# Performance work log

Measured on AMD Instinct MI355X. Metric: run time of the kernel, lower is better.

## Reference

```python
import jax, jax.numpy as jnp
import numpy as np
from jax import lax


def setup_inputs() -> dict:
    key = jax.random.key(0)
    k1, k2, k3, k4 = jax.random.split(key, 4)
    N, T = 4096, 64          # num_nodes, tokens per node
    V, H, L = 30000, 256, 2  # vocab, hidden size, LSTM layers
    data = jax.random.randint(k1, (N, T), 0, V, dtype=jnp.int64)
    embed = jax.random.uniform(k2, (V, H), jnp.float32, -0.1, 0.1)
    Wx = jax.random.normal(k3, (L, H, 4 * H), jnp.float32) * 0.05
    Wh = jax.random.normal(k4, (L, H, 4 * H), jnp.float32) * 0.05
    b = jnp.zeros((L, 4 * H), jnp.float32)
    return {"data": data, "embed": embed, "Wx": Wx, "Wh": Wh, "b": b}


def _stacked_lstm_last(tok, Wx, Wh, b):
    # tok: [N, T, H]; Wx/Wh: [L, H, 4H]; b: [L, 4H]
    L, H = Wx.shape[0], Wx.shape[1]
    N = tok.shape[0]
    xs = jnp.swapaxes(tok, 0, 1)  # [T, N, H] -- scan over time, batched over nodes
    c0 = jnp.zeros((L, N, H), tok.dtype)
    h0 = jnp.zeros((L, N, H), tok.dtype)

    def step(carry, x_t):
        c, h = carry
        inp = x_t
        new_c, new_h = [], []
        for l in range(L):  # small fixed layer loop
            z = inp @ Wx[l] + h[l] @ Wh[l] + b[l]  # [N, 4H]
            i, f, g, o = jnp.split(z, 4, axis=-1)   # flax gate order i, f, g, o
            i, f, o = jax.nn.sigmoid(i), jax.nn.sigmoid(f), jax.nn.sigmoid(o)
            g = jnp.tanh(g)
            cl = f * c[l] + i * g
            hl = o * jnp.tanh(cl)
            new_c.append(cl)
            new_h.append(hl)
            inp = hl  # top layer output feeds next layer
        return (jnp.stack(new_c), jnp.stack(new_h)), None

    (_, hF), _ = lax.scan(step, (c0, h0), xs)
    # result[-1] in the original is the top-layer output at the final step,
    # which equals the final top-layer hidden state.
    return hF[-1]  # [N, H]


def reference(data, embed, Wx, Wh, b):
    tok = embed[data]  # [N, T, H] embedding lookup
    return _stacked_lstm_last(tok, Wx, Wh, b)
```

## Files before the change

kernel.cpp:

```cpp
#include <hip/hip_runtime.h>
#include <hip/hip_bf16.h>

#define TT 64
#define HH 256
#define GG 1024

typedef _Float16 f16;
typedef __attribute__((ext_vector_type(8))) _Float16 f16x8;
typedef __attribute__((ext_vector_type(4))) _Float16 f16x4;
typedef __attribute__((ext_vector_type(4))) float f32x4;

__device__ __forceinline__ float exp2_(float x) { return __builtin_amdgcn_exp2f(x); }
__device__ __forceinline__ float sig_(float x) {
    return __builtin_amdgcn_rcpf(1.0f + exp2_(-1.44269504f * x));
}
__device__ __forceinline__ float tanh_(float x) {
    return 1.0f - 2.0f * __builtin_amdgcn_rcpf(1.0f + exp2_(2.88539008f * x));
}
__device__ __forceinline__ float sigp_(float x) { return 1.0f / (1.0f + __expf(-x)); }
__device__ __forceinline__ float tanhp_(float x) {
    x = fminf(fmaxf(x, -15.0f), 15.0f);
    float e = __expf(-2.0f * x);
    return (1.0f - e) / (1.0f + e);
}

__global__ void pack_weights(const float* __restrict__ Wx, const float* __restrict__ Wh,
                             f16* __restrict__ Wp) {
    int t = blockIdx.x * 256 + threadIdx.x;
    int lane = t & 63;
    int nt = (t >> 6) & 63;
    int kk = (t >> 12) & 15;
    int l = t >> 16;
    int n = nt * 16 + (lane & 15);
    int kbase = kk * 32 + 8 * (lane >> 4);
    const float* src = (kbase < 256) ? (Wx + (size_t)l * HH * GG + (size_t)kbase * GG + n)
                                     : (Wh + (size_t)l * HH * GG + (size_t)(kbase - 256) * GG + n);
    f16x8 v;
#pragma unroll
    for (int j = 0; j < 8; ++j) v[j] = (f16)src[(size_t)j * GG];
    *(f16x8*)(Wp + (size_t)t * 8) = v;
}

__global__ __launch_bounds__(512) void embw_gemm(
    const float* __restrict__ embed, const float* __restrict__ bias,
    const f16* __restrict__ Wp, f16* __restrict__ embW, int vocab)
{
    __shared__ f16 a_lds[32 * HH];
    const int tid = threadIdx.x;
    const int lane = tid & 63;
    const int w = tid >> 6;
    const int arow = lane & 15;
    const int g4 = lane >> 4;
    const int r0 = blockIdx.x * 32;

#pragma unroll
    for (int i = 0; i < 4; ++i) {
        int chunk = tid + i * 512;
        int row = chunk >> 6;
        int c4 = chunk & 63;
        int grow = r0 + row; if (grow >= vocab) grow = vocab - 1;
        float4 v = *(const float4*)(embed + (size_t)grow * HH + c4 * 4);
        int idx = row * HH + ((c4 * 4) ^ ((row & 7) << 3));
        *(f16x4*)&a_lds[idx] = (f16x4){(f16)v.x, (f16)v.y, (f16)v.z, (f16)v.w};
    }
    __syncthreads();

    float breg[8];
#pragma unroll
    for (int tt = 0; tt < 8; ++tt) breg[tt] = bias[(w * 8 + tt) * 16 + arow];

    f32x4 acc[2][8];
#pragma unroll
    for (int mt = 0; mt < 2; ++mt)
#pragma unroll
        for (int tt = 0; tt < 8; ++tt)
            acc[mt][tt] = (f32x4){breg[tt], breg[tt], breg[tt], breg[tt]};

    const f16* wl = Wp + (size_t)lane * 8;
#pragma unroll 2
    for (int kk = 0; kk < 8; ++kk) {
        int sw = (kk * 32 + g4 * 8) ^ ((arow & 7) << 3);
        f16x8 a0 = *(const f16x8*)&a_lds[arow * HH + sw];
        f16x8 a1 = *(const f16x8*)&a_lds[(arow + 16) * HH + sw];
        const f16* wkk = wl + (size_t)kk * 64 * 64 * 8;
#pragma unroll
        for (int tt = 0; tt < 8; ++tt) {
            f16x8 b = *(const f16x8*)(wkk + (size_t)(w * 8 + tt) * 64 * 8);
            acc[0][tt] = __builtin_amdgcn_mfma_f32_16x16x32_f16(a0, b, acc[0][tt], 0, 0, 0);
            acc[1][tt] = __builtin_amdgcn_mfma_f32_16x16x32_f16(a1, b, acc[1][tt], 0, 0, 0);
        }
    }

#pragma unroll
    for (int mt = 0; mt < 2; ++mt)
#pragma unroll
        for (int tt = 0; tt < 8; ++tt) {
            int nt = w * 8 + tt;
            int cw = (nt >> 1) & 7;
            int ctt = ((nt >> 4) << 1) | (nt & 1);
#pragma unroll
            for (int r = 0; r < 4; ++r) {
                int row = r0 + mt * 16 + g4 * 4 + r;
                if (row < vocab)
                    embW[(size_t)row * GG + cw * 128 + arow * 8 + ctt] = (f16)acc[mt][tt][r];
            }
        }
}

#define NB2 32
#define LDH 264

__global__ __launch_bounds__(512, 1) void lstm_rec2(
    const int* __restrict__ data, const float* __restrict__ bias,
    const f16* __restrict__ embW, const f16* __restrict__ Wp,
    float* __restrict__ out)
{
    __shared__ f16 h0s[2][NB2 * LDH];
    __shared__ f16 h1s[2][NB2 * LDH];
    __shared__ int toks[NB2 * TT];

    const int tid = threadIdx.x;
    const int lane = tid & 63;
    const int w = tid >> 6;
    const int arow = lane & 15;
    const int g4 = lane >> 4;
    const int n0 = blockIdx.x * NB2;

    for (int i = tid; i < NB2 * LDH; i += 512) {
        h0s[0][i] = (f16)0; h0s[1][i] = (f16)0;
        h1s[0][i] = (f16)0; h1s[1][i] = (f16)0;
    }
    for (int i = tid; i < NB2 * TT; i += 512) toks[i] = data[n0 * TT + i];

    float breg1[8];
#pragma unroll
    for (int tt = 0; tt < 8; ++tt) {
        int col = (tt >> 1) * 256 + w * 32 + (tt & 1) * 16 + arow;
        breg1[tt] = bias[GG + col];
    }

    float c0[16], c1[16];
#pragma unroll
    for (int i = 0; i < 16; ++i) { c0[i] = 0.0f; c1[i] = 0.0f; }

    const f16* wl0 = Wp + (size_t)8 * 64 * 64 * 8 + (size_t)lane * 8;
    const f16* wl1 = Wp + (size_t)16 * 64 * 64 * 8 + (size_t)lane * 8;
    const int zoff = w * 128 + arow * 8;

    int cur0 = 0, cur1 = 0;

    __syncthreads();

#pragma unroll 1
    for (int t = 0; t < TT; ++t) {
        f16x8 zfa0, zfa1, zfa2, zfa3, zfb0, zfb1, zfb2, zfb3;
        {
            int nb = g4 * 4;
            int t0 = toks[(nb + 0) * TT + t];
            int t1 = toks[(nb + 1) * TT + t];
            int t2 = toks[(nb + 2) * TT + t];
            int t3 = toks[(nb + 3) * TT + t];
            zfa0 = *(const f16x8*)(embW + (size_t)t0 * GG + zoff);
            zfa1 = *(const f16x8*)(embW + (size_t)t1 * GG + zoff);
            zfa2 = *(const f16x8*)(embW + (size_t)t2 * GG + zoff);
            zfa3 = *(const f16x8*)(embW + (size_t)t3 * GG + zoff);
        }
        {
            int nb = 16 + g4 * 4;
            int t0 = toks[(nb + 0) * TT + t];
            int t1 = toks[(nb + 1) * TT + t];
            int t2 = toks[(nb + 2) * TT + t];
            int t3 = toks[(nb + 3) * TT + t];
            zfb0 = *(const f16x8*)(embW + (size_t)t0 * GG + zoff);
            zfb1 = *(const f16x8*)(embW + (size_t)t1 * GG + zoff);
            zfb2 = *(const f16x8*)(embW + (size_t)t2 * GG + zoff);
            zfb3 = *(const f16x8*)(embW + (size_t)t3 * GG + zoff);
        }

        f32x4 acc[2][8];
#pragma unroll
        for (int mt = 0; mt < 2; ++mt)
#pragma unroll
            for (int tt = 0; tt < 8; ++tt)
                acc[mt][tt] = (f32x4){0.0f, 0.0f, 0.0f, 0.0f};

        const f16* h0cur = h0s[cur0];
#pragma unroll 2
        for (int kk = 0; kk < 8; ++kk) {
            int k0 = kk * 32 + 8 * g4;
            f16x8 a0 = *(const f16x8*)&h0cur[arow * LDH + k0];
            f16x8 a1 = *(const f16x8*)&h0cur[(arow + 16) * LDH + k0];
            const f16* wkk = wl0 + (size_t)kk * 64 * 64 * 8;
#pragma unroll
            for (int tt = 0; tt < 8; ++tt) {
                int nt = (tt >> 1) * 16 + w * 2 + (tt & 1);
                f16x8 b = *(const f16x8*)(wkk + (size_t)nt * 64 * 8);
                acc[0][tt] = __builtin_amdgcn_mfma_f32_16x16x32_f16(a0, b, acc[0][tt], 0, 0, 0);
                acc[1][tt] = __builtin_amdgcn_mfma_f32_16x16x32_f16(a1, b, acc[1][tt], 0, 0, 0);
            }
        }

#pragma unroll
        for (int tt = 0; tt < 8; ++tt) {
            acc[0][tt][0] += (float)zfa0[tt];
            acc[0][tt][1] += (float)zfa1[tt];
            acc[0][tt][2] += (float)zfa2[tt];
            acc[0][tt][3] += (float)zfa3[tt];
            acc[1][tt][0] += (float)zfb0[tt];
            acc[1][tt][1] += (float)zfb1[tt];
            acc[1][tt][2] += (float)zfb2[tt];
            acc[1][tt][3] += (float)zfb3[tt];
        }

        f16* h0new = h0s[cur0 ^ 1];
#pragma unroll
        for (int mt = 0; mt < 2; ++mt)
#pragma unroll
            for (int sub = 0; sub < 2; ++sub)
#pragma unroll
                for (int r = 0; r < 4; ++r) {
                    int node = mt * 16 + g4 * 4 + r;
                    float i_ = sig_(acc[mt][0 + sub][r]);
                    float f_ = sig_(acc[mt][2 + sub][r]);
                    float g_ = tanh_(acc[mt][4 + sub][r]);
                    float o_ = sig_(acc[mt][6 + sub][r]);
                    int ci = mt * 8 + sub * 4 + r;
                    float c = fmaf(f_, c0[ci], i_ * g_);
                    c0[ci] = c;
                    int u = w * 32 + sub * 16 + arow;
                    h0new[node * LDH + u] = (f16)(o_ * tanh_(c));
                }
        __syncthreads();

        f32x4 acc1[2][8];
#pragma unroll
        for (int mt = 0; mt < 2; ++mt)
#pragma unroll
            for (int tt = 0; tt < 8; ++tt)
                acc1[mt][tt] = (f32x4){breg1[tt], breg1[tt], breg1[tt], breg1[tt]};

        const f16* h1cur = h1s[cur1];
#pragma unroll 4
        for (int kk = 0; kk < 16; ++kk) {
            const f16* asrc = (kk < 8) ? (const f16*)h0new : h1cur;
            int k0 = (kk & 7) * 32 + 8 * g4;
            f16x8 a0 = *(const f16x8*)&asrc[arow * LDH + k0];
            f16x8 a1 = *(const f16x8*)&asrc[(arow + 16) * LDH + k0];
            const f16* wkk = wl1 + (size_t)kk * 64 * 64 * 8;
#pragma unroll
            for (int tt = 0; tt < 8; ++tt) {
                int nt = (tt >> 1) * 16 + w * 2 + (tt & 1);
                f16x8 b = *(const f16x8*)(wkk + (size_t)nt * 64 * 8);
                acc1[0][tt] = __builtin_amdgcn_mfma_f32_16x16x32_f16(a0, b, acc1[0][tt], 0, 0, 0);
                acc1[1][tt] = __builtin_amdgcn_mfma_f32_16x16x32_f16(a1, b, acc1[1][tt], 0, 0, 0);
            }
        }

#pragma unroll
        for (int mt = 0; mt < 2; ++mt)
#pragma unroll
            for (int sub = 0; sub < 2; ++sub)
#pragma unroll
                for (int r = 0; r < 4; ++r) {
                    int node = mt * 16 + g4 * 4 + r;
                    float i_ = sig_(acc1[mt][0 + sub][r]);
                    float f_ = sig_(acc1[mt][2 + sub][r]);
                    float g_ = tanh_(acc1[mt][4 + sub][r]);
                    float o_ = sig_(acc1[mt][6 + sub][r]);
                    int ci = mt * 8 + sub * 4 + r;
                    float c = fmaf(f_, c1[ci], i_ * g_);
                    c1[ci] = c;
                    int u = w * 32 + sub * 16 + arow;
                    h1s[cur1 ^ 1][node * LDH + u] = (f16)(o_ * tanh_(c));
                }
        cur0 ^= 1;
        cur1 ^= 1;
    }
    __syncthreads();

    for (int i = tid; i < NB2 * HH; i += 512) {
        int n = i >> 8, k = i & 255;
        out[(size_t)(n0 + n) * HH + k] = (float)h1s[cur1][n * LDH + k];
    }
}

__global__ void convert_embed(const float* __restrict__ e, f16* __restrict__ o, int n8) {
    int i = blockIdx.x * 256 + threadIdx.x;
    if (i >= n8) return;
    size_t p = (size_t)i * 8;
    float4 a = *(const float4*)(e + p);
    float4 b = *(const float4*)(e + p + 4);
    f16x8 v = { (f16)a.x, (f16)a.y, (f16)a.z, (f16)a.w,
                (f16)b.x, (f16)b.y, (f16)b.z, (f16)b.w };
    *(f16x8*)(o + p) = v;
}

#define FB 32
#define FTH 512
#define FLD 264
__device__ __forceinline__ void fb_layer_step(
    const f16 (*bx)[FLD], f16 (*bh)[FLD], const f16* __restrict__ wlayer,
    const float* breg_l, float* c_l, int lane, int w)
{
    f32x4 acc[2][8];
#pragma unroll
    for (int mt = 0; mt < 2; ++mt)
#pragma unroll
        for (int tt = 0; tt < 8; ++tt) {
            float b = breg_l[tt];
            acc[mt][tt] = (f32x4){b, b, b, b};
        }
    const int arow = lane & 15;
    const int koff = 8 * (lane >> 4);
    const f16* wl = wlayer + (size_t)lane * 8;
#pragma unroll 2
    for (int kk = 0; kk < 16; ++kk) {
        int k0 = (kk & 7) * 32 + koff;
        const f16(*src)[FLD] = (kk < 8) ? bx : (const f16(*)[FLD])bh;
        f16x8 a0 = *(const f16x8*)&src[arow][k0];
        f16x8 a1 = *(const f16x8*)&src[arow + 16][k0];
        const f16* wkk = wl + (size_t)kk * 64 * 64 * 8;
#pragma unroll
        for (int tt = 0; tt < 8; ++tt) {
            int nt = (tt >> 1) * 16 + w * 2 + (tt & 1);
            f16x8 b = *(const f16x8*)(wkk + (size_t)nt * 64 * 8);
            acc[0][tt] = __builtin_amdgcn_mfma_f32_16x16x32_f16(a0, b, acc[0][tt], 0, 0, 0);
            acc[1][tt] = __builtin_amdgcn_mfma_f32_16x16x32_f16(a1, b, acc[1][tt], 0, 0, 0);
        }
    }
    __syncthreads();
#pragma unroll
    for (int mt = 0; mt < 2; ++mt)
#pragma unroll
        for (int sub = 0; sub < 2; ++sub) {
            f32x4 iv = acc[mt][0 + sub], fv = acc[mt][2 + sub];
            f32x4 gv = acc[mt][4 + sub], ov = acc[mt][6 + sub];
#pragma unroll
            for (int r = 0; r < 4; ++r) {
                float i_ = sigp_(iv[r]), f_ = sigp_(fv[r]), g_ = tanhp_(gv[r]), o_ = sigp_(ov[r]);
                int ci = mt * 8 + sub * 4 + r;
                float c = fmaf(f_, c_l[ci], i_ * g_);
                c_l[ci] = c;
                int node = mt * 16 + (lane >> 4) * 4 + r;
                int unit = w * 32 + sub * 16 + (lane & 15);
                bh[node][unit] = (f16)(o_ * tanhp_(c));
            }
        }
    __syncthreads();
}

__global__ __launch_bounds__(FTH, 2) void lstm_mfma_fb(
    const int* __restrict__ data, const float* __restrict__ bias,
    const f16* __restrict__ emb, const f16* __restrict__ Wp,
    float* __restrict__ out, int vocab)
{
    __shared__ f16 x_lds[FB][FLD];
    __shared__ f16 h0_lds[FB][FLD];
    __shared__ f16 h1_lds[FB][FLD];
    const int tid = threadIdx.x;
    const int lane = tid & 63;
    const int w = tid >> 6;
    const int n0 = blockIdx.x * FB;
    for (int i = tid; i < FB * FLD; i += FTH) {
        (&h0_lds[0][0])[i] = (f16)0.0f; (&h1_lds[0][0])[i] = (f16)0.0f;
    }
    float breg[2][8];
#pragma unroll
    for (int l = 0; l < 2; ++l)
#pragma unroll
        for (int tt = 0; tt < 8; ++tt) {
            int col = (tt >> 1) * 256 + w * 32 + (tt & 1) * 16 + (lane & 15);
            breg[l][tt] = bias[l * GG + col];
        }
    float cst[2][16];
#pragma unroll
    for (int i = 0; i < 32; ++i) (&cst[0][0])[i] = 0.0f;
    __syncthreads();
    const f16* Wp0 = Wp;
    const f16* Wp1 = Wp + (size_t)16 * 64 * 64 * 8;
    for (int t = 0; t < TT; ++t) {
        {
            int n = tid >> 4;
            int cg = (tid & 15) * 16;
            int row = data[(n0 + n) * TT + t];
            row = min(max(row, 0), vocab - 1);
            const f16* src = emb + (size_t)row * HH + cg;
            *(f16x8*)&x_lds[n][cg] = *(const f16x8*)src;
            *(f16x8*)&x_lds[n][cg + 8] = *(const f16x8*)(src + 8);
        }
        __syncthreads();
        fb_layer_step(x_lds, h0_lds, Wp0, breg[0], cst[0], lane, w);
        fb_layer_step((const f16(*)[FLD])h0_lds, h1_lds, Wp1, breg[1], cst[1], lane, w);
    }
    for (int i = tid; i < FB * HH; i += FTH) {
        int n = i >> 8, k = i & 255;
        out[(size_t)(n0 + n) * HH + k] = (float)h1_lds[n][k];
    }
}

extern "C" void kernel_launch(void* const* d_in, const int* in_sizes, int n_in,
                              void* d_out, int out_size, void* d_ws, size_t ws_size,
                              hipStream_t stream) {
    const int* data = (const int*)d_in[0];
    const float* embed = (const float*)d_in[1];
    const float* Wx = (const float*)d_in[2];
    const float* Wh = (const float*)d_in[3];
    const float* bias = (const float*)d_in[4];
    float* out = (float*)d_out;
    const int vocab = in_sizes[1] / HH;
    const int nNodes = in_sizes[0] / TT;

    const size_t wp_bytes = (size_t)2 * 16 * 64 * 64 * 8 * 2;
    const size_t embw_bytes = (size_t)vocab * GG * 2;
    const size_t emb16_bytes = (size_t)vocab * HH * 2;

    if (ws_size >= embw_bytes + wp_bytes) {
        f16* embW = (f16*)d_ws;
        f16* Wp = (f16*)((char*)d_ws + embw_bytes);
        pack_weights<<<dim3(512), dim3(256), 0, stream>>>(Wx, Wh, Wp);
        embw_gemm<<<dim3((vocab + 31) / 32), dim3(512), 0, stream>>>(embed, bias, Wp, embW, vocab);
        lstm_rec2<<<dim3(nNodes / NB2), dim3(512), 0, stream>>>(data, bias, embW, Wp, out);
        return;
    }
    f16* emb_h = (f16*)d_ws;
    f16* Wp = (f16*)((char*)d_ws + emb16_bytes);
    int n8 = in_sizes[1] / 8;
    convert_embed<<<dim3((n8 + 255) / 256), dim3(256), 0, stream>>>(embed, emb_h, n8);
    pack_weights<<<dim3(512), dim3(256), 0, stream>>>(Wx, Wh, Wp);
    lstm_mfma_fb<<<dim3(nNodes / FB), dim3(FTH), 0, stream>>>(data, bias, emb_h, Wp, out, vocab);
}
```

Baseline: 1.113 ms.

## Double recurrent kernel threads to 1024 and split gate columns across wave pairs

The recurrent LSTM kernel now launches 16 waves per block instead of 8. Each wave pair splits the former 32-unit slice by sub-half, so every wave holds 4 accumulator tiles instead of 8 and keeps half as much cell state. The packed embedding-projection layout in the precompute GEMM is reordered so each wave reads a contiguous 4-element f16 chunk of its gate preactivations. The aim is more latency hiding and MFMA issue parallelism on the sequential time loop. The cost is more waves sharing the same LDS h tiles and barriers, and twice the A-operand LDS reads per block.

```diff
diff --git a/kernel.cpp b/kernel.cpp
--- a/kernel.cpp
+++ b/kernel.cpp
@@ -97,7 +97,7 @@
         for (int tt = 0; tt < 8; ++tt) {
             int nt = w * 8 + tt;
             int cw = (nt >> 1) & 7;
-            int ctt = ((nt >> 4) << 1) | (nt & 1);
+            int ctt = ((nt & 1) << 2) | (nt >> 4);
 #pragma unroll
             for (int r = 0; r < 4; ++r) {
                 int row = r0 + mt * 16 + g4 * 4 + r;
@@ -109,8 +109,9 @@
 
 #define NB2 32
 #define LDH 264
-
-__global__ __launch_bounds__(512, 1) void lstm_rec2(
+#define RTH 1024
+
+__global__ __launch_bounds__(RTH, 1) void lstm_rec2(
     const int* __restrict__ data, const float* __restrict__ bias,
     const f16* __restrict__ embW, const f16* __restrict__ Wp,
     float* __restrict__ out)
@@ -122,30 +123,30 @@
     const int tid = threadIdx.x;
     const int lane = tid & 63;
     const int w = tid >> 6;
+    const int wq = w >> 1;
+    const int sub = w & 1;
     const int arow = lane & 15;
     const int g4 = lane >> 4;
     const int n0 = blockIdx.x * NB2;
 
-    for (int i = tid; i < NB2 * LDH; i += 512) {
+    for (int i = tid; i < NB2 * LDH; i += RTH) {
         h0s[0][i] = (f16)0; h0s[1][i] = (f16)0;
         h1s[0][i] = (f16)0; h1s[1][i] = (f16)0;
     }
-    for (int i = tid; i < NB2 * TT; i += 512) toks[i] = data[n0 * TT + i];
-
-    float breg1[8];
-#pragma unroll
-    for (int tt = 0; tt < 8; ++tt) {
-        int col = (tt >> 1) * 256 + w * 32 + (tt & 1) * 16 + arow;
-        breg1[tt] = bias[GG + col];
-    }
-
-    float c0[16], c1[16];
-#pragma unroll
-    for (int i = 0; i < 16; ++i) { c0[i] = 0.0f; c1[i] = 0.0f; }
-
-    const f16* wl0 = Wp + (size_t)8 * 64 * 64 * 8 + (size_t)lane * 8;
-    const f16* wl1 = Wp + (size_t)16 * 64 * 64 * 8 + (size_t)lane * 8;
-    const int zoff = w * 128 + arow * 8;
+    for (int i = tid; i < NB2 * TT; i += RTH) toks[i] = data[n0 * TT + i];
+
+    const int u = wq * 32 + sub * 16 + arow;
+    float breg1[4];
+#pragma unroll
+    for (int g = 0; g < 4; ++g) breg1[g] = bias[GG + g * 256 + u];
+
+    float c0[8], c1[8];
+#pragma unroll
+    for (int i = 0; i < 8; ++i) { c0[i] = 0.0f; c1[i] = 0.0f; }
+
+    const f16* wl0 = Wp + (size_t)8 * 32768 + (size_t)lane * 8;
+    const f16* wl1 = Wp + (size_t)16 * 32768 + (size_t)lane * 8;
+    const int zoff = wq * 128 + arow * 8 + sub * 4;
 
     int cur0 = 0, cur1 = 0;
 
@@ -153,17 +154,17 @@
 
 #pragma unroll 1
     for (int t = 0; t < TT; ++t) {
-        f16x8 zfa0, zfa1, zfa2, zfa3, zfb0, zfb1, zfb2, zfb3;
+        f16x4 zfa0, zfa1, zfa2, zfa3, zfb0, zfb1, zfb2, zfb3;
         {
             int nb = g4 * 4;
             int t0 = toks[(nb + 0) * TT + t];
             int t1 = toks[(nb + 1) * TT + t];
             int t2 = toks[(nb + 2) * TT + t];
             int t3 = toks[(nb + 3) * TT + t];
-            zfa0 = *(const f16x8*)(embW + (size_t)t0 * GG + zoff);
-            zfa1 = *(const f16x8*)(embW + (size_t)t1 * GG + zoff);
-            zfa2 = *(const f16x8*)(embW + (size_t)t2 * GG + zoff);
-            zfa3 = *(const f16x8*)(embW + (size_t)t3 * GG + zoff);
+            zfa0 = *(const f16x4*)(embW + (size_t)t0 * GG + zoff);
+            zfa1 = *(const f16x4*)(embW + (size_t)t1 * GG + zoff);
+            zfa2 = *(const f16x4*)(embW + (size_t)t2 * GG + zoff);
+            zfa3 = *(const f16x4*)(embW + (size_t)t3 * GG + zoff);
         }
         {
             int nb = 16 + g4 * 4;
@@ -171,73 +172,69 @@
             int t1 = toks[(nb + 1) * TT + t];
             int t2 = toks[(nb + 2) * TT + t];
             int t3 = toks[(nb + 3) * TT + t];
-            zfb0 = *(const f16x8*)(embW + (size_t)t0 * GG + zoff);
-            zfb1 = *(const f16x8*)(embW + (size_t)t1 * GG + zoff);
-            zfb2 = *(const f16x8*)(embW + (size_t)t2 * GG + zoff);
-            zfb3 = *(const f16x8*)(embW + (size_t)t3 * GG + zoff);
-        }
-
-        f32x4 acc[2][8];
+            zfb0 = *(const f16x4*)(embW + (size_t)t0 * GG + zoff);
+            zfb1 = *(const f16x4*)(embW + (size_t)t1 * GG + zoff);
+            zfb2 = *(const f16x4*)(embW + (size_t)t2 * GG + zoff);
+            zfb3 = *(const f16x4*)(embW + (size_t)t3 * GG + zoff);
+        }
+
+        f32x4 acc[2][4];
 #pragma unroll
         for (int mt = 0; mt < 2; ++mt)
 #pragma unroll
-            for (int tt = 0; tt < 8; ++tt)
-                acc[mt][tt] = (f32x4){0.0f, 0.0f, 0.0f, 0.0f};
+            for (int g = 0; g < 4; ++g)
+                acc[mt][g] = (f32x4){0.0f, 0.0f, 0.0f, 0.0f};
 
         const f16* h0cur = h0s[cur0];
-#pragma unroll 2
+#pragma unroll
         for (int kk = 0; kk < 8; ++kk) {
             int k0 = kk * 32 + 8 * g4;
             f16x8 a0 = *(const f16x8*)&h0cur[arow * LDH + k0];
             f16x8 a1 = *(const f16x8*)&h0cur[(arow + 16) * LDH + k0];
-            const f16* wkk = wl0 + (size_t)kk * 64 * 64 * 8;
-#pragma unroll
-            for (int tt = 0; tt < 8; ++tt) {
-                int nt = (tt >> 1) * 16 + w * 2 + (tt & 1);
-                f16x8 b = *(const f16x8*)(wkk + (size_t)nt * 64 * 8);
-                acc[0][tt] = __builtin_amdgcn_mfma_f32_16x16x32_f16(a0, b, acc[0][tt], 0, 0, 0);
-                acc[1][tt] = __builtin_amdgcn_mfma_f32_16x16x32_f16(a1, b, acc[1][tt], 0, 0, 0);
-            }
-        }
-
-#pragma unroll
-        for (int tt = 0; tt < 8; ++tt) {
-            acc[0][tt][0] += (float)zfa0[tt];
-            acc[0][tt][1] += (float)zfa1[tt];
-            acc[0][tt][2] += (float)zfa2[tt];
-            acc[0][tt][3] += (float)zfa3[tt];
-            acc[1][tt][0] += (float)zfb0[tt];
-            acc[1][tt][1] += (float)zfb1[tt];
-            acc[1][tt][2] += (float)zfb2[tt];
-            acc[1][tt][3] += (float)zfb3[tt];
+            const f16* wkk = wl0 + (size_t)kk * 32768;
+#pragma unroll
+            for (int g = 0; g < 4; ++g) {
+                f16x8 b = *(const f16x8*)(wkk + (size_t)(g * 16 + wq * 2 + sub) * 512);
+                acc[0][g] = __builtin_amdgcn_mfma_f32_16x16x32_f16(a0, b, acc[0][g], 0, 0, 0);
+                acc[1][g] = __builtin_amdgcn_mfma_f32_16x16x32_f16(a1, b, acc[1][g], 0, 0, 0);
+            }
+        }
+
+#pragma unroll
+        for (int g = 0; g < 4; ++g) {
+            acc[0][g][0] += (float)zfa0[g];
+            acc[0][g][1] += (float)zfa1[g];
+            acc[0][g][2] += (float)zfa2[g];
+            acc[0][g][3] += (float)zfa3[g];
+            acc[1][g][0] += (float)zfb0[g];
+            acc[1][g][1] += (float)zfb1[g];
+            acc[1][g][2] += (float)zfb2[g];
+            acc[1][g][3] += (float)zfb3[g];
         }
 
         f16* h0new = h0s[cur0 ^ 1];
 #pragma unroll
         for (int mt = 0; mt < 2; ++mt)
 #pragma unroll
-            for (int sub = 0; sub < 2; ++sub)
-#pragma unroll
-                for (int r = 0; r < 4; ++r) {
-                    int node = mt * 16 + g4 * 4 + r;
-                    float i_ = sig_(acc[mt][0 + sub][r]);
-                    float f_ = sig_(acc[mt][2 + sub][r]);
-                    float g_ = tanh_(acc[mt][4 + sub][r]);
-                    float o_ = sig_(acc[mt][6 + sub][r]);
-                    int ci = mt * 8 + sub * 4 + r;
-                    float c = fmaf(f_, c0[ci], i_ * g_);
-                    c0[ci] = c;
-                    int u = w * 32 + sub * 16 + arow;
-                    h0new[node * LDH + u] = (f16)(o_ * tanh_(c));
-                }
+            for (int r = 0; r < 4; ++r) {
+                int node = mt * 16 + g4 * 4 + r;
+                float i_ = sig_(acc[mt][0][r]);
+                float f_ = sig_(acc[mt][1][r]);
+                float g_ = tanh_(acc[mt][2][r]);
+                float o_ = sig_(acc[mt][3][r]);
+                int ci = mt * 4 + r;
+                float c = fmaf(f_, c0[ci], i_ * g_);
+                c0[ci] = c;
+                h0new[node * LDH + u] = (f16)(o_ * tanh_(c));
+            }
         __syncthreads();
 
-        f32x4 acc1[2][8];
+        f32x4 acc1[2][4];
 #pragma unroll
         for (int mt = 0; mt < 2; ++mt)
 #pragma unroll
-            for (int tt = 0; tt < 8; ++tt)
-                acc1[mt][tt] = (f32x4){breg1[tt], breg1[tt], breg1[tt], breg1[tt]};
+            for (int g = 0; g < 4; ++g)
+                acc1[mt][g] = (f32x4){breg1[g], breg1[g], breg1[g], breg1[g]};
 
         const f16* h1cur = h1s[cur1];
 #pragma unroll 4
@@ -246,39 +243,35 @@
             int k0 = (kk & 7) * 32 + 8 * g4;
             f16x8 a0 = *(const f16x8*)&asrc[arow * LDH + k0];
             f16x8 a1 = *(const f16x8*)&asrc[(arow + 16) * LDH + k0];
-            const f16* wkk = wl1 + (size_t)kk * 64 * 64 * 8;
-#pragma unroll
-            for (int tt = 0; tt < 8; ++tt) {
-                int nt = (tt >> 1) * 16 + w * 2 + (tt & 1);
-                f16x8 b = *(const f16x8*)(wkk + (size_t)nt * 64 * 8);
-                acc1[0][tt] = __builtin_amdgcn_mfma_f32_16x16x32_f16(a0, b, acc1[0][tt], 0, 0, 0);
-                acc1[1][tt] = __builtin_amdgcn_mfma_f32_16x16x32_f16(a1, b, acc1[1][tt], 0, 0, 0);
+            const f16* wkk = wl1 + (size_t)kk * 32768;
+#pragma unroll
+            for (int g = 0; g < 4; ++g) {
+                f16x8 b = *(const f16x8*)(wkk + (size_t)(g * 16 + wq * 2 + sub) * 512);
+                acc1[0][g] = __builtin_amdgcn_mfma_f32_16x16x32_f16(a0, b, acc1[0][g], 0, 0, 0);
+                acc1[1][g] = __builtin_amdgcn_mfma_f32_16x16x32_f16(a1, b, acc1[1][g], 0, 0, 0);
             }
         }
 
 #pragma unroll
         for (int mt = 0; mt < 2; ++mt)
 #pragma unroll
-            for (int sub = 0; sub < 2; ++sub)
-#pragma unroll
-                for (int r = 0; r < 4; ++r) {
-                    int node = mt * 16 + g4 * 4 + r;
-                    float i_ = sig_(acc1[mt][0 + sub][r]);
-                    float f_ = sig_(acc1[mt][2 + sub][r]);
-                    float g_ = tanh_(acc1[mt][4 + sub][r]);
-                    float o_ = sig_(acc1[mt][6 + sub][r]);
-                    int ci = mt * 8 + sub * 4 + r;
-                    float c = fmaf(f_, c1[ci], i_ * g_);
-                    c1[ci] = c;
-                    int u = w * 32 + sub * 16 + arow;
-                    h1s[cur1 ^ 1][node * LDH + u] = (f16)(o_ * tanh_(c));
-                }
+            for (int r = 0; r < 4; ++r) {
+                int node = mt * 16 + g4 * 4 + r;
+                float i_ = sig_(acc1[mt][0][r]);
+                float f_ = sig_(acc1[mt][1][r]);
+                float g_ = tanh_(acc1[mt][2][r]);
+                float o_ = sig_(acc1[mt][3][r]);
+                int ci = mt * 4 + r;
+                float c = fmaf(f_, c1[ci], i_ * g_);
+                c1[ci] = c;
+                h1s[cur1 ^ 1][node * LDH + u] = (f16)(o_ * tanh_(c));
+            }
         cur0 ^= 1;
         cur1 ^= 1;
     }
     __syncthreads();
 
-    for (int i = tid; i < NB2 * HH; i += 512) {
+    for (int i = tid; i < NB2 * HH; i += RTH) {
         int n = i >> 8, k = i & 255;
         out[(size_t)(n0 + n) * HH + k] = (float)h1s[cur1][n * LDH + k];
     }
@@ -419,7 +412,7 @@
         f16* Wp = (f16*)((char*)d_ws + embw_bytes);
         pack_weights<<<dim3(512), dim3(256), 0, stream>>>(Wx, Wh, Wp);
         embw_gemm<<<dim3((vocab + 31) / 32), dim3(512), 0, stream>>>(embed, bias, Wp, embW, vocab);
-        lstm_rec2<<<dim3(nNodes / NB2), dim3(512), 0, stream>>>(data, bias, embW, Wp, out);
+        lstm_rec2<<<dim3(nNodes / NB2), dim3(RTH), 0, stream>>>(data, bias, embW, Wp, out);
         return;
     }
     f16* emb_h = (f16*)d_ws;
```

New measurement: 2.217 ms. 99.2% more time.
